# Optimization experiments

Hardware: AMD Instinct MI355X
Metric: run time of the kernel (lower is better)

Reference implementation:

```python
import jax, jax.numpy as jnp
import numpy as np

ALPHA = 0.2  # LeakyReLU negative slope
NUM_HEADS, OUT_DIM = 8, 16
N_NODES, N_EDGES, IN_DIM = 50000, 800000, 128


def setup_inputs() -> dict:
    key = jax.random.key(0)
    k = jax.random.split(key, 6)
    return {
        "x": jax.random.normal(k[0], (N_NODES, IN_DIM), dtype=jnp.float32),
        "W1": jax.random.normal(k[1], (IN_DIM, IN_DIM), dtype=jnp.float32) * (1.414 / np.sqrt(IN_DIM)),
        "W2": jax.random.normal(k[2], (NUM_HEADS * OUT_DIM, IN_DIM), dtype=jnp.float32) * (1.414 / np.sqrt(IN_DIM)),
        "attn_l": jax.random.normal(k[3], (NUM_HEADS, OUT_DIM), dtype=jnp.float32) * 0.3,
        "attn_r": jax.random.normal(k[4], (NUM_HEADS, OUT_DIM), dtype=jnp.float32) * 0.3,
        "edge_index": jax.random.randint(k[5], (2, N_EDGES), 0, N_NODES, dtype=jnp.int64),
    }


def reference(x, W1, W2, attn_l, attn_r, edge_index):
    N = x.shape[0]
    H, D = attn_l.shape
    # fc1 -> leaky_relu -> fc2, reshape to per-head features [N, H, D]
    h2 = jax.nn.leaky_relu(x @ W1.T, ALPHA)
    ft = (h2 @ W2.T).reshape(N, H, D)
    # per-node attention halves: a1 = ft . attn_l, a2 = ft . attn_r  -> [N, H]
    a1 = jnp.einsum('nhd,hd->nh', ft, attn_l)
    a2 = jnp.einsum('nhd,hd->nh', ft, attn_r)
    src, dst = edge_index[0], edge_index[1]
    # edge attention logits [E, H]
    e = jax.nn.leaky_relu(a1[src] + a2[dst], ALPHA)
    # edge softmax normalized over incoming edges of each dst node
    emax = jax.ops.segment_max(e, dst, num_segments=N)
    ee = jnp.exp(e - emax[dst])
    esum = jax.ops.segment_sum(ee, dst, num_segments=N)
    a = ee / esum[dst]  # [E, H]
    # weighted scatter-sum aggregation: sum_{e: dst(e)=n} a_e * ft[src(e)]
    msg = ft[src] * a[:, :, None]  # [E, H, D]
    out = jax.ops.segment_sum(msg, dst, num_segments=N)  # [N, H, D]
    return out
```

## Files before the change

### kernel.cpp

```cpp
#include <hip/hip_runtime.h>

#define ALPHA 0.2f
constexpr int N = 50000;
constexpr int E = 800000;

typedef __attribute__((ext_vector_type(8))) short bf16x8;
typedef __attribute__((ext_vector_type(4))) float f32x4;

__device__ inline ushort f2bf(float v) {
  uint u = __float_as_uint(v);
  return (ushort)((u + 0x7fff + ((u >> 16) & 1)) >> 16);
}
__device__ inline float bf2f(ushort u) { return __uint_as_float(((uint)u) << 16); }

constexpr int LDX = 136;

constexpr int BN   = 128;
constexpr int NB   = (N + BN - 1) / BN;
constexpr int NBP  = 512;
constexpr int PSTR = 392;
constexpr int CHUNK = 4096;
constexpr int NBLK  = (E + CHUNK - 1) / CHUNK;
constexpr int FROWS = 32;
constexpr int FEATB = (N + FROWS - 1) / FROWS;
constexpr int SMEMB = 2 * FROWS * LDX * 2;

__global__ __launch_bounds__(256) void k1_kernel(const float* __restrict__ W1,
    const float* __restrict__ W2, ushort* __restrict__ wf1hi, ushort* __restrict__ wf1lo,
    ushort* __restrict__ wf2hi, ushort* __restrict__ wf2lo,
    const int* __restrict__ dst, int* __restrict__ partial) {
  const int bid = blockIdx.x;
  const int t = threadIdx.x;
  if (bid < NBLK) {
    __shared__ int lh[NB];
    const int e0 = bid * CHUNK, e1 = min(e0 + CHUNK, E);
    for (int i = t; i < NB; i += 256) lh[i] = 0;
    __syncthreads();
    for (int i = e0 + t; i < e1; i += 256)
      atomicAdd(&lh[((unsigned)dst[i]) >> 7], 1);
    __syncthreads();
    for (int i = t; i < NB; i += 256) partial[bid * PSTR + i] = lh[i];
    return;
  }
  int g = (bid - NBLK) * 256 + t;
  const float* W = (g < 2048) ? W1 : W2;
  ushort* whi = (g < 2048) ? wf1hi : wf2hi;
  ushort* wlo = (g < 2048) ? wf1lo : wf2lo;
  int f = g & 2047;
  int ks = f >> 9, rem = f & 511, jb = rem >> 6, l = rem & 63;
  int m = jb * 16 + (l & 15), kb = ks * 32 + (l >> 4) * 8;
#pragma unroll
  for (int q = 0; q < 2; ++q) {
    float4 v = *(const float4*)&W[m * 128 + kb + q * 4];
    ushort4 hi, lo;
    hi.x = f2bf(v.x); lo.x = f2bf(v.x - bf2f(hi.x));
    hi.y = f2bf(v.y); lo.y = f2bf(v.y - bf2f(hi.y));
    hi.z = f2bf(v.z); lo.z = f2bf(v.z - bf2f(hi.z));
    hi.w = f2bf(v.w); lo.w = f2bf(v.w - bf2f(hi.w));
    *(ushort4*)&whi[f * 8 + q * 4] = hi;
    *(ushort4*)&wlo[f * 8 + q * 4] = lo;
  }
}

__global__ __launch_bounds__(NBP) void colscan_kernel(const int* __restrict__ partial,
    int* __restrict__ bucket_base, int* __restrict__ chunk_base) {
  __shared__ int sh[NBP];
  const int t = threadIdx.x;
  int tot = 0;
  if (t < NB) {
#pragma unroll 4
    for (int blk = 0; blk < NBLK; ++blk) tot += partial[blk * PSTR + t];
  }
  sh[t] = (t < NB) ? tot : 0;
  __syncthreads();
  for (int off = 1; off < NBP; off <<= 1) {
    int u = (t >= off) ? sh[t - off] : 0;
    __syncthreads();
    sh[t] += u;
    __syncthreads();
  }
  if (t < NB) {
    int base = sh[t] - tot;
    bucket_base[t] = base;
    int run = base;
#pragma unroll 4
    for (int blk = 0; blk < NBLK; ++blk) {
      chunk_base[blk * PSTR + t] = run;
      run += partial[blk * PSTR + t];
    }
  }
  if (t == NB - 1) bucket_base[NB] = sh[t];
}

__global__ __launch_bounds__(256, 6) void featpart_kernel(
    const float* __restrict__ x,
    const ushort* __restrict__ wf1hi, const ushort* __restrict__ wf1lo,
    const ushort* __restrict__ wf2hi, const ushort* __restrict__ wf2lo,
    const float* __restrict__ attn_l, const float* __restrict__ attn_r,
    ushort* __restrict__ ft_bf, float* __restrict__ a1, float* __restrict__ a2,
    const int* __restrict__ src, const int* __restrict__ dst,
    const int* __restrict__ chunk_base, int* __restrict__ ebuf) {
  extern __shared__ char smem[];
  const int bid = blockIdx.x;
  const int tid = threadIdx.x;

  if (bid < NBLK) {
    int* curs = (int*)smem;
    const int e0 = bid * CHUNK, e1 = min(e0 + CHUNK, E);
    for (int k = tid; k < NB; k += 256) curs[k] = chunk_base[bid * PSTR + k];
    __syncthreads();
    for (int i = e0 + tid; i < e1; i += 256) {
      int s = src[i], d = dst[i];
      int pos = atomicAdd(&curs[((unsigned)d) >> 7], 1);
      ebuf[pos] = (s << 7) | (d & 127);
    }
    return;
  }

  ushort* sXhi = (ushort*)smem;
  ushort* sXlo = sXhi + FROWS * LDX;
  const int w = tid >> 6, l = tid & 63;
  const int lr = l & 15, lg4 = l >> 4;
  const int rowBase = (bid - NBLK) * FROWS;

  for (int i = tid; i < FROWS * 32; i += 256) {
    int row = i >> 5, kc = i & 31;
    int g = rowBase + row;
    float4 v = make_float4(0.f, 0.f, 0.f, 0.f);
    if (g < N) v = reinterpret_cast<const float4*>(x)[g * 32 + kc];
    ushort4 hi, lo;
    hi.x = f2bf(v.x); lo.x = f2bf(v.x - bf2f(hi.x));
    hi.y = f2bf(v.y); lo.y = f2bf(v.y - bf2f(hi.y));
    hi.z = f2bf(v.z); lo.z = f2bf(v.z - bf2f(hi.z));
    hi.w = f2bf(v.w); lo.w = f2bf(v.w - bf2f(hi.w));
    *(ushort4*)&sXhi[row * LDX + kc * 4] = hi;
    *(ushort4*)&sXlo[row * LDX + kc * 4] = lo;
  }
  __syncthreads();

  f32x4 acc[2][2];
#pragma unroll
  for (int mi = 0; mi < 2; ++mi)
#pragma unroll
    for (int jj = 0; jj < 2; ++jj) acc[mi][jj] = (f32x4){0.f, 0.f, 0.f, 0.f};

#pragma unroll
  for (int ks = 0; ks < 4; ++ks) {
    bf16x8 bh[2], bl[2], ah[2], al[2];
#pragma unroll
    for (int jj = 0; jj < 2; ++jj) {
      int off = ((ks * 8 + (2 * w + jj)) * 64 + l) * 8;
      bh[jj] = *(const bf16x8*)&wf1hi[off];
      bl[jj] = *(const bf16x8*)&wf1lo[off];
    }
#pragma unroll
    for (int mi = 0; mi < 2; ++mi) {
      int addr = (mi * 16 + lr) * LDX + ks * 32 + lg4 * 8;
      ah[mi] = *(const bf16x8*)&sXhi[addr];
      al[mi] = *(const bf16x8*)&sXlo[addr];
    }
#pragma unroll
    for (int mi = 0; mi < 2; ++mi)
#pragma unroll
      for (int jj = 0; jj < 2; ++jj) {
        acc[mi][jj] = __builtin_amdgcn_mfma_f32_16x16x32_bf16(ah[mi], bh[jj], acc[mi][jj], 0, 0, 0);
        acc[mi][jj] = __builtin_amdgcn_mfma_f32_16x16x32_bf16(ah[mi], bl[jj], acc[mi][jj], 0, 0, 0);
        acc[mi][jj] = __builtin_amdgcn_mfma_f32_16x16x32_bf16(al[mi], bh[jj], acc[mi][jj], 0, 0, 0);
      }
  }
  __syncthreads();

#pragma unroll
  for (int mi = 0; mi < 2; ++mi)
#pragma unroll
    for (int jj = 0; jj < 2; ++jj)
#pragma unroll
      for (int r = 0; r < 4; ++r) {
        float v = acc[mi][jj][r];
        v = v > 0.f ? v : ALPHA * v;
        int row = mi * 16 + lg4 * 4 + r;
        int col = w * 32 + jj * 16 + lr;
        ushort hv = f2bf(v);
        sXhi[row * LDX + col] = hv;
        sXlo[row * LDX + col] = f2bf(v - bf2f(hv));
      }
  __syncthreads();

#pragma unroll
  for (int mi = 0; mi < 2; ++mi)
#pragma unroll
    for (int jj = 0; jj < 2; ++jj) acc[mi][jj] = (f32x4){0.f, 0.f, 0.f, 0.f};

#pragma unroll
  for (int ks = 0; ks < 4; ++ks) {
    bf16x8 bh[2], bl[2], ah[2], al[2];
#pragma unroll
    for (int jj = 0; jj < 2; ++jj) {
      int off = ((ks * 8 + (2 * w + jj)) * 64 + l) * 8;
      bh[jj] = *(const bf16x8*)&wf2hi[off];
      bl[jj] = *(const bf16x8*)&wf2lo[off];
    }
#pragma unroll
    for (int mi = 0; mi < 2; ++mi) {
      int addr = (mi * 16 + lr) * LDX + ks * 32 + lg4 * 8;
      ah[mi] = *(const bf16x8*)&sXhi[addr];
      al[mi] = *(const bf16x8*)&sXlo[addr];
    }
#pragma unroll
    for (int mi = 0; mi < 2; ++mi)
#pragma unroll
      for (int jj = 0; jj < 2; ++jj) {
        acc[mi][jj] = __builtin_amdgcn_mfma_f32_16x16x32_bf16(ah[mi], bh[jj], acc[mi][jj], 0, 0, 0);
        acc[mi][jj] = __builtin_amdgcn_mfma_f32_16x16x32_bf16(ah[mi], bl[jj], acc[mi][jj], 0, 0, 0);
        acc[mi][jj] = __builtin_amdgcn_mfma_f32_16x16x32_bf16(al[mi], bh[jj], acc[mi][jj], 0, 0, 0);
      }
  }

#pragma unroll
  for (int mi = 0; mi < 2; ++mi)
#pragma unroll
    for (int jj = 0; jj < 2; ++jj) {
      int h = 2 * w + jj;
      float alv = attn_l[h * 16 + lr], arv = attn_r[h * 16 + lr];
#pragma unroll
      for (int r = 0; r < 4; ++r) {
        float v = acc[mi][jj][r];
        int grow = rowBase + mi * 16 + lg4 * 4 + r;
        bool valid = grow < N;
        if (valid) ft_bf[grow * 128 + h * 16 + lr] = f2bf(v);
        float sl = v * alv, sr = v * arv;
#pragma unroll
        for (int off = 8; off; off >>= 1) {
          sl += __shfl_xor(sl, off, 16);
          sr += __shfl_xor(sr, off, 16);
        }
        if (valid && lr == 0) { a1[grow * 8 + h] = sl; a2[grow * 8 + h] = sr; }
      }
    }
}

__global__ __launch_bounds__(256) void fine_kernel(const int* __restrict__ ebuf,
    const int* __restrict__ bucket_base, int* __restrict__ row_ptr,
    int* __restrict__ col_src) {
  __shared__ int ldeg[BN], curs[BN];
  __shared__ int w0tot;
  const int b = blockIdx.x, t = threadIdx.x;
  const int node0 = b * BN;
  const int nloc = min(BN, N - node0);
  const int bstart = bucket_base[b], bend = bucket_base[b + 1];
  if (t < BN) ldeg[t] = 0;
  __syncthreads();
  for (int i = bstart + t; i < bend; i += 256)
    atomicAdd(&ldeg[ebuf[i] & 127], 1);
  __syncthreads();
  int v = (t < BN) ? ldeg[t] : 0;
  int sc = v;
#pragma unroll
  for (int off = 1; off < 64; off <<= 1) {
    int u = __shfl_up(sc, off, 64);
    if ((t & 63) >= off) sc += u;
  }
  if (t == 63) w0tot = sc;
  __syncthreads();
  int excl = sc - v + ((t >= 64 && t < BN) ? w0tot : 0);
  if (t < nloc) {
    int base = bstart + excl;
    row_ptr[node0 + t] = base;
    curs[t] = base;
  }
  if (b == NB - 1 && t == 0) row_ptr[N] = bend;
  __syncthreads();
  for (int i = bstart + t; i < bend; i += 256) {
    int pr = ebuf[i];
    int pos = atomicAdd(&curs[pr & 127], 1);
    col_src[pos] = pr >> 7;
  }
}

__global__ __launch_bounds__(256) void agg_kernel(const int* __restrict__ row_ptr,
    const int* __restrict__ col_src, const ushort* __restrict__ ft_bf,
    const float* __restrict__ a1, const float* __restrict__ a2,
    float* __restrict__ out) {
  const int node = blockIdx.x * 4 + (threadIdx.x >> 6);
  if (node >= N) return;
  const int t = threadIdx.x & 63;
  const int eSlot = t >> 3;
  const int hA = t & 7;
  const int hB = t >> 3;
  const int start = row_ptr[node], end = row_ptr[node + 1];
  const float a2nA = a2[node * 8 + hA];

  float l = 0.f, acc0 = 0.f, acc1 = 0.f;
  if (end > start) {
    int rem = min(end - start, 8);
    int idx = start + (eSlot < rem ? eSlot : rem - 1);
    int sA = col_src[idx];
    float lg = a1[sA * 8 + hA] + a2nA;
    lg = lg > 0.f ? lg : ALPHA * lg;
    float pA = (eSlot < rem) ? __expf(lg) : 0.f;

    for (int base = start; base < end; base += 8) {
      int nbase = base + 8;
      int sN = 0; float pN = 0.f;
      if (nbase < end) {
        int rem2 = min(end - nbase, 8);
        int idx2 = nbase + (eSlot < rem2 ? eSlot : rem2 - 1);
        sN = col_src[idx2];
        float lg2 = a1[sN * 8 + hA] + a2nA;
        lg2 = lg2 > 0.f ? lg2 : ALPHA * lg2;
        pN = (eSlot < rem2) ? __expf(lg2) : 0.f;
      }
#pragma unroll
      for (int e = 0; e < 8; ++e) {
        float pe = __shfl(pA, e * 8 + hB);
        int se = __shfl(sA, e * 8);
        ushort2 f = *(const ushort2*)&ft_bf[se * 128 + t * 2];
        l += pe;
        acc0 = fmaf(pe, bf2f(f.x), acc0);
        acc1 = fmaf(pe, bf2f(f.y), acc1);
      }
      sA = sN; pA = pN;
    }
  }
  float inv = (end > start) ? 1.f / l : 0.f;
  *(float2*)&out[node * 128 + t * 2] = make_float2(acc0 * inv, acc1 * inv);
}

extern "C" void kernel_launch(void* const* d_in, const int* in_sizes, int n_in,
                              void* d_out, int out_size, void* d_ws, size_t ws_size,
                              hipStream_t stream) {
  const float* x      = (const float*)d_in[0];
  const float* W1     = (const float*)d_in[1];
  const float* W2     = (const float*)d_in[2];
  const float* attn_l = (const float*)d_in[3];
  const float* attn_r = (const float*)d_in[4];
  const int*   edge   = (const int*)d_in[5];
  const int*   src    = edge;
  const int*   dst    = edge + E;
  float* out = (float*)d_out;

  char* ws = (char*)d_ws;
  ushort* ft_bf       = (ushort*)(ws);
  float*  a1          = (float*) (ws + 12800000);
  float*  a2          = (float*) (ws + 14400000);
  int*    row_ptr     = (int*)   (ws + 16000000);
  int*    bucket_base = (int*)   (ws + 16200064);
  int*    col_src     = (int*)   (ws + 16201664);
  ushort* wf1hi       = (ushort*)(ws + 19401664);
  ushort* wf1lo       = (ushort*)(ws + 19434432);
  ushort* wf2hi       = (ushort*)(ws + 19467200);
  ushort* wf2lo       = (ushort*)(ws + 19499968);
  int*    ebuf        = (int*)   (ws + 19532736);
  int*    partial     = (int*)   (ws + 22732736);
  int*    chunk_base  = (int*)   (ws + 23040064);

  k1_kernel<<<NBLK + 16, 256, 0, stream>>>(W1, W2, wf1hi, wf1lo, wf2hi, wf2lo, dst, partial);
  colscan_kernel<<<1, NBP, 0, stream>>>(partial, bucket_base, chunk_base);
  featpart_kernel<<<NBLK + FEATB, 256, SMEMB, stream>>>(
      x, wf1hi, wf1lo, wf2hi, wf2lo, attn_l, attn_r, ft_bf, a1, a2,
      src, dst, chunk_base, ebuf);
  fine_kernel<<<NB, 256, 0, stream>>>(ebuf, bucket_base, row_ptr, col_src);
  agg_kernel<<<(N + 3) / 4, 256, 0, stream>>>(row_ptr, col_src, ft_bf, a1, a2, out);
}
```

Baseline: 110.9 us.

## Gather neighbor features with 16-byte loads across quarter-wave edge groups

The aggregation kernel reassigns work within each wavefront. Each group of 16 lanes now handles one edge at a time, and each lane loads 8 bf16 features in a single 16-byte load instead of every lane loading 2 features for every edge. The four lane groups process different edges in parallel and are combined at the end with xor-shuffle reductions before a float4 store. The software prefetch of the next edge batch's indices and logits is dropped, which simplifies the loop but may expose load latency on nodes with many incoming edges.

```diff
diff --git a/kernel.cpp b/kernel.cpp
--- a/kernel.cpp
+++ b/kernel.cpp
@@ -6,6 +6,7 @@
 
 typedef __attribute__((ext_vector_type(8))) short bf16x8;
 typedef __attribute__((ext_vector_type(4))) float f32x4;
+typedef __attribute__((ext_vector_type(8))) unsigned short ush8;
 
 __device__ inline ushort f2bf(float v) {
   uint u = __float_as_uint(v);
@@ -286,44 +287,46 @@
   const int t = threadIdx.x & 63;
   const int eSlot = t >> 3;
   const int hA = t & 7;
-  const int hB = t >> 3;
+  const int q = t >> 4;
+  const int c = t & 15;
   const int start = row_ptr[node], end = row_ptr[node + 1];
   const float a2nA = a2[node * 8 + hA];
 
-  float l = 0.f, acc0 = 0.f, acc1 = 0.f;
-  if (end > start) {
-    int rem = min(end - start, 8);
-    int idx = start + (eSlot < rem ? eSlot : rem - 1);
-    int sA = col_src[idx];
-    float lg = a1[sA * 8 + hA] + a2nA;
+  float l = 0.f;
+  float acc8[8];
+#pragma unroll
+  for (int v = 0; v < 8; ++v) acc8[v] = 0.f;
+
+  for (int base = start; base < end; base += 8) {
+    int rem = end - base; rem = rem > 8 ? 8 : rem;
+    int idx = base + (eSlot < rem ? eSlot : rem - 1);
+    int s = col_src[idx];
+    float lg = a1[s * 8 + hA] + a2nA;
     lg = lg > 0.f ? lg : ALPHA * lg;
-    float pA = (eSlot < rem) ? __expf(lg) : 0.f;
-
-    for (int base = start; base < end; base += 8) {
-      int nbase = base + 8;
-      int sN = 0; float pN = 0.f;
-      if (nbase < end) {
-        int rem2 = min(end - nbase, 8);
-        int idx2 = nbase + (eSlot < rem2 ? eSlot : rem2 - 1);
-        sN = col_src[idx2];
-        float lg2 = a1[sN * 8 + hA] + a2nA;
-        lg2 = lg2 > 0.f ? lg2 : ALPHA * lg2;
-        pN = (eSlot < rem2) ? __expf(lg2) : 0.f;
-      }
-#pragma unroll
-      for (int e = 0; e < 8; ++e) {
-        float pe = __shfl(pA, e * 8 + hB);
-        int se = __shfl(sA, e * 8);
-        ushort2 f = *(const ushort2*)&ft_bf[se * 128 + t * 2];
-        l += pe;
-        acc0 = fmaf(pe, bf2f(f.x), acc0);
-        acc1 = fmaf(pe, bf2f(f.y), acc1);
-      }
-      sA = sN; pA = pN;
-    }
+    float p = (eSlot < rem) ? __expf(lg) : 0.f;
+#pragma unroll
+    for (int k = 0; k < 2; ++k) {
+      int eb = 4 * k + q;
+      float pe = __shfl(p, eb * 8 + (c >> 1));
+      int se = __shfl(s, eb * 8);
+      ush8 f = *(const ush8*)&ft_bf[se * 128 + c * 8];
+      l += pe;
+#pragma unroll
+      for (int v = 0; v < 8; ++v) acc8[v] = fmaf(pe, bf2f(f[v]), acc8[v]);
+    }
+  }
+#pragma unroll
+  for (int off = 16; off <= 32; off <<= 1) {
+    l += __shfl_xor(l, off);
+#pragma unroll
+    for (int v = 0; v < 8; ++v) acc8[v] += __shfl_xor(acc8[v], off);
   }
   float inv = (end > start) ? 1.f / l : 0.f;
-  *(float2*)&out[node * 128 + t * 2] = make_float2(acc0 * inv, acc1 * inv);
+  if (t < 32) {
+    float4 o = make_float4(acc8[q * 4 + 0] * inv, acc8[q * 4 + 1] * inv,
+                           acc8[q * 4 + 2] * inv, acc8[q * 4 + 3] * inv);
+    *(float4*)&out[node * 128 + c * 8 + q * 4] = o;
+  }
 }
 
 extern "C" void kernel_launch(void* const* d_in, const int* in_sizes, int n_in,
```

Measured after the change: 110.9 us. About the same (+0.0%).
